# Optimization experiments

Hardware: AMD Instinct MI355X
Metric: run time of the kernel (lower is better)

## Reference

```python
import jax, jax.numpy as jnp
import numpy as np

N, E, G = 2048, 65536, 32
F_ATOM, LAT, IN, ED, NB, L = 16, 64, 128, 32, 5, 5


def setup_inputs() -> dict:
    key = jax.random.key(0)
    ks = iter(jax.random.split(key, 64))
    nxt = lambda: next(ks)
    def w(shape):
        fan_in = shape[-2] if len(shape) >= 2 else 1
        return jax.random.normal(nxt(), shape, jnp.float32) / np.sqrt(fan_in)
    inp = {}
    inp['x'] = jax.random.normal(nxt(), (N, F_ATOM), jnp.float32)
    inp['t'] = jax.random.uniform(nxt(), (G, 1), jnp.float32)
    inp['z'] = jax.random.normal(nxt(), (N, LAT), jnp.float32)
    inp['edge_index'] = jax.random.randint(nxt(), (2, E), 0, N, jnp.int32)
    inp['edge_attr'] = jax.random.normal(nxt(), (E, NB), jnp.float32)
    inp['batch'] = jnp.sort(jax.random.randint(nxt(), (N,), 0, G, jnp.int32))
    inp['batch_edge_global'] = jax.random.randint(nxt(), (E,), 0, G, jnp.int32)
    # top-level dense layers
    inp['Wt_a'] = w((1, IN)); inp['bt_a'] = jnp.zeros((IN,))
    inp['Wt_b'] = w((1, ED)); inp['bt_b'] = jnp.zeros((ED,))
    inp['W_atom'] = w((F_ATOM, IN)); inp['b_atom'] = jnp.zeros((IN,))
    inp['W_bond'] = w((NB, ED)); inp['b_bond'] = jnp.zeros((ED,))
    inp['W_lat'] = w((LAT, IN)); inp['b_lat'] = jnp.zeros((IN,))
    inp['W_at'] = w((IN, IN)); inp['b_at'] = jnp.zeros((IN,))
    inp['W_bt'] = w((ED, ED)); inp['b_bt'] = jnp.zeros((ED,))
    # TopoEdgeGNN: L layers of edge-conditioned message passing with edge update
    inp['Wmsg'] = w((L, 2 * IN + ED, IN)); inp['bmsg'] = jnp.zeros((L, IN))
    inp['Wnode'] = w((L, 2 * IN, IN)); inp['bnode'] = jnp.zeros((L, IN))
    inp['Wedge'] = w((L, 2 * IN + ED, ED)); inp['bedge'] = jnp.zeros((L, ED))
    # prediction head
    inp['Wsh'] = w((IN, IN)); inp['bsh'] = jnp.zeros((IN,))
    inp['Wbm'] = w((ED, IN)); inp['bbm'] = jnp.zeros((IN,))
    inp['Wbl'] = w((IN, NB)); inp['bbl'] = jnp.zeros((NB,))
    inp['Wal'] = w((IN, F_ATOM + LAT)); inp['bal'] = jnp.zeros((F_ATOM + LAT,))
    return inp


def reference(x, t, z, edge_index, edge_attr, batch, batch_edge_global,
              Wt_a, bt_a, Wt_b, bt_b, W_atom, b_atom, W_bond, b_bond,
              W_lat, b_lat, W_at, b_at, W_bt, b_bt,
              Wmsg, bmsg, Wnode, bnode, Wedge, bedge,
              Wsh, bsh, Wbm, bbm, Wbl, bbl, Wal, bal):
    j, i = edge_index[0], edge_index[1]
    # time embeddings, gathered to nodes / edges
    ta = t @ Wt_a + bt_a            # [G, IN]
    tb = t @ Wt_b + bt_b            # [G, ED]
    tnode = ta[batch]               # [N, IN]
    tedge = tb[batch_edge_global]   # [E, ED]
    # node features
    s = x @ W_atom + b_atom
    s = (s + tnode) @ W_at + b_at
    s = s + (z @ W_lat + b_lat)
    # edge features
    e = edge_attr @ W_bond + b_bond
    e = (e + tedge) @ W_bt + b_bt
    # TopoEdgeGNN: message passing with residual node/edge updates
    for l in range(L):
        m = jax.nn.silu(jnp.concatenate([s[i], s[j], e], -1) @ Wmsg[l] + bmsg[l])  # [E, IN]
        agg = jax.ops.segment_sum(m, i, num_segments=N)                            # [N, IN]
        s = s + jax.nn.silu(jnp.concatenate([s, agg], -1) @ Wnode[l] + bnode[l])
        e = e + jax.nn.silu(jnp.concatenate([s[i], s[j], e], -1) @ Wedge[l] + bedge[l])
    # prediction head
    s2 = jax.nn.silu(s @ Wsh + bsh)
    al = s2 @ Wal + bal
    atoms_pred, latent_pred = al[:, :F_ATOM], al[:, F_ATOM:]
    # dense edge symmetrization: scatter edges into [N, N, ED], symmetrize, gather back
    e_dense = jnp.zeros((N, N, ED), e.dtype).at[j, i].set(e)
    e_dense = 0.5 * (e_dense + e_dense.transpose(1, 0, 2))
    e_sym = e_dense[j, i]           # [E, ED]
    f = jax.nn.silu(s2[i] + s2[j] + (e_sym @ Wbm + bbm))
    bonds_pred = f @ Wbl + bbl
    return latent_pred, atoms_pred, bonds_pred
```

## Files before the change

### kernel.cpp

```cpp
#include <hip/hip_runtime.h>
#include <hip/hip_bf16.h>

#define NN 2048
#define NE 65536
#define NG 32
#define CIN 128
#define CED 32
#define CLAT 64
#define CFA 16
#define CNB 5
#define NL 5

#define OFF_AT (NN * CLAT)
#define OFF_B  (NN * CLAT + NN * CFA)

typedef __attribute__((ext_vector_type(8))) short bf16x8;
typedef __attribute__((ext_vector_type(4))) float f32x4;

__device__ __forceinline__ float silu_f(float v) { return v / (1.0f + __expf(-v)); }
__device__ __forceinline__ short f2bs(float v) {
    __hip_bfloat16 h = __float2bfloat16(v);
    return *reinterpret_cast<short*>(&h);
}
__device__ __forceinline__ float bs2f(short s) {
    return __bfloat162float(*reinterpret_cast<__hip_bfloat16*>(&s));
}
__device__ __forceinline__ unsigned pack2(float a, float b) {
    return ((unsigned)(unsigned short)f2bs(b) << 16) | (unsigned short)f2bs(a);
}
__device__ __forceinline__ unsigned addpack(unsigned ua, unsigned va) {
    float a0 = bs2f((short)(ua & 0xffff)), a1 = bs2f((short)(ua >> 16));
    float b0 = bs2f((short)(va & 0xffff)), b1 = bs2f((short)(va >> 16));
    return pack2(a0 + b0, a1 + b1);
}

struct KArgs {
    const float *x, *t, *z;
    const int *jj, *ii;
    const float *ea;
    const int *batch, *beg;
    const float *Wt_a, *bt_a, *Wt_b, *bt_b, *W_atom, *b_atom, *W_bond, *b_bond;
    const float *W_lat, *b_lat, *W_at, *b_at, *W_bt, *b_bt;
    const float *Wmsg, *bmsg, *Wnode, *bnode, *Wedge, *bedge;
    const float *Wsh, *bsh, *Wbm, *bbm, *Wbl, *bbl, *Wal, *bal;
    float *s, *e;
    float *agg;
    int *cnt, *rowpos, *rowstart, *invp, *i_s, *j_s;
    short *s2, *U, *V, *P, *Q;
    int *map;
    short *Wpn, *Wpsh, *Wpal, *Wpbm, *Wproj, *W3m, *We3;
    int *gsync;
    float *out;
};

__device__ __forceinline__ void gbar(int* gs)
{
    __syncthreads();
    if (threadIdx.x == 0) {
        __threadfence();
        int g = __hip_atomic_load(gs + 32, __ATOMIC_RELAXED, __HIP_MEMORY_SCOPE_AGENT);
        int* gc = gs + 64 + ((blockIdx.x >> 5) << 5);
        if (__hip_atomic_fetch_add(gc, 1, __ATOMIC_ACQ_REL, __HIP_MEMORY_SCOPE_AGENT) == 31) {
            __hip_atomic_store(gc, 0, __ATOMIC_RELAXED, __HIP_MEMORY_SCOPE_AGENT);
            if (__hip_atomic_fetch_add(gs, 1, __ATOMIC_ACQ_REL, __HIP_MEMORY_SCOPE_AGENT) == 31) {
                __hip_atomic_store(gs, 0, __ATOMIC_RELAXED, __HIP_MEMORY_SCOPE_AGENT);
                __hip_atomic_store(gs + 32, g + 1, __ATOMIC_RELEASE, __HIP_MEMORY_SCOPE_AGENT);
            }
        }
        while (__hip_atomic_load(gs + 32, __ATOMIC_RELAXED, __HIP_MEMORY_SCOPE_AGENT) == g)
            __builtin_amdgcn_s_sleep(8);
    }
    __syncthreads();
    __threadfence();
}

__device__ __forceinline__ void phase_pack(const KArgs& a, int start, int stride)
{
    for (int idx = start; idx < 6 * 4 * 20 * 64 * 8; idx += stride) {
        int j = idx & 7, t0 = idx >> 3, lane = t0 & 63, tt = t0 >> 6;
        int kq = (lane >> 4) * 8 + j, n16 = lane & 15;
        if (idx < NL * 8 * 8 * 64 * 8) {
            int nt = tt & 7, kt = (tt >> 3) & 7, l = tt >> 6;
            a.Wpn[idx] = f2bs(a.Wnode[((size_t)l * 256 + kt * 32 + kq) * CIN + nt * 16 + n16]);
        }
        if (idx < 4 * 8 * 64 * 8) {
            int nt = tt & 7, kt = tt >> 3;
            a.Wpsh[idx] = f2bs(a.Wsh[(size_t)(kt * 32 + kq) * CIN + nt * 16 + n16]);
        }
        if (idx < 4 * 5 * 64 * 8) {
            int nt = tt % 5, kt = tt / 5;
            a.Wpal[idx] = f2bs(a.Wal[(size_t)(kt * 32 + kq) * 80 + nt * 16 + n16]);
        }
        if (idx < 8 * 64 * 8) {
            int nt = tt & 7;
            a.Wpbm[idx] = f2bs(a.Wbm[(size_t)kq * CIN + nt * 16 + n16]);
        }
        {
            int nt = tt % 20; int t2 = tt / 20; int kt = t2 & 3; int slot = t2 >> 2;
            int k = kt * 32 + kq;
            float v;
            if (nt < 16) {
                int msgl = slot % 5;
                int srcK = (nt < 8) ? k : 128 + k;
                int col = (nt & 7) * 16 + n16;
                v = a.Wmsg[((size_t)msgl * 288 + srcK) * CIN + col];
            } else {
                int edgel = (slot == 0) ? 0 : slot - 1;
                int srcK = (nt < 18) ? k : 128 + k;
                int col = (nt & 1) * 16 + n16;
                v = a.Wedge[((size_t)edgel * 288 + srcK) * CED + col];
            }
            a.Wproj[idx] = f2bs(v);
        }
        if (idx < NL * 8 * 64 * 8) {
            int nt = tt & 7, l = tt >> 3;
            a.W3m[idx] = f2bs(a.Wmsg[((size_t)l * 288 + 256 + kq) * CIN + nt * 16 + n16]);
        }
        if (idx < NL * 2 * 64 * 8) {
            int nt = tt & 1, l = tt >> 1;
            a.We3[idx] = f2bs(a.Wedge[((size_t)l * 288 + 256 + kq) * CED + nt * 16 + n16]);
        }
    }
}

__device__ __forceinline__ void phase_init_s(const KArgs& a, char* smem, int tile, int tid)
{
    float* xs  = (float*)smem;
    float* zs  = (float*)(smem + 1024);
    float* tmp = (float*)(smem + 5120);
    float* tv  = (float*)(smem + 13312);
    int nb0 = tile * 16;
    int c = tid & 127, h = tid >> 7;
    if (tid < 16 * CFA / 4) ((float4*)xs)[tid] = ((const float4*)a.x)[nb0 * (CFA / 4) + tid];
    if (tid < 16 * CLAT / 4) ((float4*)zs)[tid] = ((const float4*)a.z)[nb0 * (CLAT / 4) + tid];
    if (tid < 16) tv[tid] = a.t[a.batch[nb0 + tid]];
    __syncthreads();
    float wta = a.Wt_a[c], base0 = a.b_atom[c] + a.bt_a[c];
    float acc[8];
#pragma unroll
    for (int q = 0; q < 8; q++) acc[q] = base0 + tv[h * 8 + q] * wta;
    for (int k = 0; k < CFA; k++) {
        float w = a.W_atom[k * CIN + c];
#pragma unroll
        for (int q = 0; q < 8; q++) acc[q] += xs[(h * 8 + q) * CFA + k] * w;
    }
#pragma unroll
    for (int q = 0; q < 8; q++) tmp[(h * 8 + q) * CIN + c] = acc[q];
    __syncthreads();
    float base1 = a.b_at[c] + a.b_lat[c];
    float acc2[8];
#pragma unroll
    for (int q = 0; q < 8; q++) acc2[q] = base1;
    for (int k4 = 0; k4 < CIN / 4; k4++) {
        float w0 = a.W_at[(4 * k4 + 0) * CIN + c], w1 = a.W_at[(4 * k4 + 1) * CIN + c];
        float w2 = a.W_at[(4 * k4 + 2) * CIN + c], w3 = a.W_at[(4 * k4 + 3) * CIN + c];
#pragma unroll
        for (int q = 0; q < 8; q++) {
            float4 f = *(const float4*)&tmp[(h * 8 + q) * CIN + 4 * k4];
            acc2[q] += f.x * w0 + f.y * w1 + f.z * w2 + f.w * w3;
        }
    }
    for (int k4 = 0; k4 < CLAT / 4; k4++) {
        float w0 = a.W_lat[(4 * k4 + 0) * CIN + c], w1 = a.W_lat[(4 * k4 + 1) * CIN + c];
        float w2 = a.W_lat[(4 * k4 + 2) * CIN + c], w3 = a.W_lat[(4 * k4 + 3) * CIN + c];
#pragma unroll
        for (int q = 0; q < 8; q++) {
            float4 f = *(const float4*)&zs[(h * 8 + q) * CLAT + 4 * k4];
            acc2[q] += f.x * w0 + f.y * w1 + f.z * w2 + f.w * w3;
        }
    }
#pragma unroll
    for (int q = 0; q < 8; q++) {
        int nd = nb0 + h * 8 + q;
        a.s[(size_t)nd * CIN + c] = acc2[q];
    }
}

__device__ __forceinline__ void phase_init_e(const KArgs& a, char* smem, int tb, int tid)
{
    float* eas   = (float*)smem;
    float* tv    = (float*)(smem + 1280);
    int*   sp    = (int*)(smem + 1536);
    float* tmp   = (float*)(smem + 1792);
    float* wbt   = (float*)(smem + 10240);
    float* wbond = (float*)(smem + 14336);
    float* cb    = (float*)(smem + 14976);
    float* wtb   = (float*)(smem + 15104);
    float* bbt2  = (float*)(smem + 15232);
    int k0 = tb * 64;
    for (int idx = tid; idx < 320; idx += 256) eas[idx] = a.ea[(size_t)k0 * 5 + idx];
    if (tid < 64) { tv[tid] = a.t[a.beg[k0 + tid]]; sp[tid] = a.invp[k0 + tid]; }
    for (int idx = tid; idx < 1024; idx += 256) wbt[idx] = a.W_bt[idx];
    if (tid < 160) wbond[tid] = a.W_bond[tid];
    if (tid < 32) { cb[tid] = a.b_bond[tid] + a.bt_b[tid]; wtb[tid] = a.Wt_b[tid]; bbt2[tid] = a.b_bt[tid]; }
    __syncthreads();
    int ch = tid & 31, eg = tid >> 5;
#pragma unroll
    for (int q = 0; q < 8; q++) {
        int le = eg * 8 + q;
        float acc = cb[ch] + tv[le] * wtb[ch];
#pragma unroll
        for (int bb = 0; bb < CNB; bb++) acc += eas[le * 5 + bb] * wbond[bb * 32 + ch];
        tmp[le * 33 + ch] = acc;
    }
    __syncthreads();
#pragma unroll
    for (int q = 0; q < 8; q++) {
        int le = eg * 8 + q;
        float acc2 = bbt2[ch];
        for (int d = 0; d < 32; d++) acc2 += tmp[le * 33 + d] * wbt[d * 32 + ch];
        size_t ix = (size_t)sp[le] * CED + ch;
        a.e[ix] = acc2;
        if (ch == 0) {
            int k = k0 + le;
            atomicMax(&a.map[(size_t)a.jj[k] * NN + a.ii[k]], k);
        }
    }
}

__device__ __forceinline__ void phase_node2(
    const KArgs& a, char* smem, int tile, int tid, bool DO_NODE, bool DO_POST,
    bool LOAD_S, bool STORE_S,
    const short* Wpn_l, const float* bnode_l, const short* Wproj_slot, float (*s_reg)[4])
{
    short* feat  = (short*)smem;
    short* feat2 = (short*)(smem + 8448);
    int nb0 = tile * 16;
    int lane = tid & 63, w = tid >> 6;
    int quad = lane >> 4, n16 = lane & 15;

    if (DO_NODE) {
#pragma unroll
        for (int n2 = 0; n2 < 2; n2++) {
            int col = (w * 2 + n2) * 16 + n16;
#pragma unroll
            for (int r = 0; r < 4; r++) {
                int row = quad * 4 + r;
                if (LOAD_S) s_reg[n2][r] = a.s[(size_t)(nb0 + row) * CIN + col];
                feat[row * 264 + col] = f2bs(s_reg[n2][r]);
            }
        }
#pragma unroll
        for (int k2 = 0; k2 < 2; k2++) {
            int idx = tid + k2 * 256;
            int kl = idx >> 5, c = idx & 31;
            size_t base = (size_t)(nb0 + kl) * 128 + c;
            float4 p0 = ((const float4*)a.agg)[base];
            float4 p1 = ((const float4*)a.agg)[base + 32];
            float4 p2 = ((const float4*)a.agg)[base + 64];
            float4 p3 = ((const float4*)a.agg)[base + 96];
            float4 z4 = {0.f, 0.f, 0.f, 0.f};
            ((float4*)a.agg)[base] = z4;
            ((float4*)a.agg)[base + 32] = z4;
            ((float4*)a.agg)[base + 64] = z4;
            ((float4*)a.agg)[base + 96] = z4;
            float4 v; v.x = p0.x + p1.x + p2.x + p3.x; v.y = p0.y + p1.y + p2.y + p3.y;
            v.z = p0.z + p1.z + p2.z + p3.z; v.w = p0.w + p1.w + p2.w + p3.w;
            uint2 p; p.x = pack2(v.x, v.y); p.y = pack2(v.z, v.w);
            *(uint2*)&feat[kl * 264 + 128 + 4 * c] = p;
        }
        __syncthreads();
        f32x4 acc[2];
        acc[0] = (f32x4){0.f, 0.f, 0.f, 0.f};
        acc[1] = (f32x4){0.f, 0.f, 0.f, 0.f};
        const short* fbase = feat + n16 * 264 + quad * 8;
#pragma unroll
        for (int kt = 0; kt < 8; kt++) {
            bf16x8 av = *(const bf16x8*)(fbase + kt * 32);
#pragma unroll
            for (int n2 = 0; n2 < 2; n2++) {
                int nt = w * 2 + n2;
                bf16x8 b = *(const bf16x8*)(Wpn_l + ((size_t)(kt * 8 + nt) * 64 + lane) * 8);
                acc[n2] = __builtin_amdgcn_mfma_f32_16x16x32_bf16(av, b, acc[n2], 0, 0, 0);
            }
        }
#pragma unroll
        for (int n2 = 0; n2 < 2; n2++) {
            int col = (w * 2 + n2) * 16 + n16;
            float bb = bnode_l[col];
#pragma unroll
            for (int r = 0; r < 4; r++) {
                int row = quad * 4 + r;
                float v = s_reg[n2][r] + silu_f(acc[n2][r] + bb);
                s_reg[n2][r] = v;
                if (STORE_S) a.s[(size_t)(nb0 + row) * CIN + col] = v;
                feat2[row * 136 + col] = f2bs(v);
            }
        }
        __syncthreads();
    } else {
        int kl = tid >> 4, c = tid & 15;
        const float4* sp4 = (const float4*)&a.s[(size_t)(nb0 + kl) * CIN + c * 8];
        float4 v0 = sp4[0], v1 = sp4[1];
        uint4 p; p.x = pack2(v0.x, v0.y); p.y = pack2(v0.z, v0.w);
        p.z = pack2(v1.x, v1.y); p.w = pack2(v1.z, v1.w);
        *(uint4*)&feat2[kl * 136 + c * 8] = p;
        __syncthreads();
    }

    {
        f32x4 accp[5];
#pragma unroll
        for (int t2 = 0; t2 < 5; t2++) accp[t2] = (f32x4){0.f, 0.f, 0.f, 0.f};
        const short* abase = feat2 + n16 * 136 + quad * 8;
#pragma unroll
        for (int kt = 0; kt < 4; kt++) {
            bf16x8 av = *(const bf16x8*)(abase + kt * 32);
#pragma unroll
            for (int n5 = 0; n5 < 5; n5++) {
                int nt = w * 5 + n5;
                bf16x8 b = *(const bf16x8*)(Wproj_slot + ((size_t)(kt * 20 + nt) * 64 + lane) * 8);
                accp[n5] = __builtin_amdgcn_mfma_f32_16x16x32_bf16(av, b, accp[n5], 0, 0, 0);
            }
        }
#pragma unroll
        for (int n5 = 0; n5 < 5; n5++) {
            int nt = w * 5 + n5;
#pragma unroll
            for (int r = 0; r < 4; r++) {
                int node = tile * 16 + quad * 4 + r;
                short bv = f2bs(accp[n5][r]);
                if (nt < 8)       a.U[(size_t)node * CIN + nt * 16 + n16] = bv;
                else if (nt < 16) a.V[(size_t)node * CIN + (nt - 8) * 16 + n16] = bv;
                else if (nt < 18) a.P[(size_t)node * CED + (nt - 16) * 16 + n16] = bv;
                else              a.Q[(size_t)node * CED + (nt - 18) * 16 + n16] = bv;
            }
        }
    }

    if (DO_POST) {
        short* feat_s2 = feat;
        const short* fbase = feat2 + n16 * 136 + quad * 8;
        f32x4 acc[2];
        acc[0] = (f32x4){0.f, 0.f, 0.f, 0.f};
        acc[1] = (f32x4){0.f, 0.f, 0.f, 0.f};
#pragma unroll
        for (int kt = 0; kt < 4; kt++) {
            bf16x8 av = *(const bf16x8*)(fbase + kt * 32);
#pragma unroll
            for (int n2 = 0; n2 < 2; n2++) {
                int nt = w * 2 + n2;
                bf16x8 b = *(const bf16x8*)(a.Wpsh + ((size_t)(kt * 8 + nt) * 64 + lane) * 8);
                acc[n2] = __builtin_amdgcn_mfma_f32_16x16x32_bf16(av, b, acc[n2], 0, 0, 0);
            }
        }
#pragma unroll
        for (int n2 = 0; n2 < 2; n2++) {
            int col = (w * 2 + n2) * 16 + n16;
            float bb = a.bsh[col];
#pragma unroll
            for (int r = 0; r < 4; r++) {
                int row = quad * 4 + r;
                float v = silu_f(acc[n2][r] + bb);
                short bv = f2bs(v);
                a.s2[(size_t)(nb0 + row) * CIN + col] = bv;
                feat_s2[row * 136 + col] = bv;
            }
        }
        __syncthreads();
        const short* abase2 = feat_s2 + n16 * 136 + quad * 8;
        f32x4 acca[2];
        acca[0] = (f32x4){0.f, 0.f, 0.f, 0.f};
        acca[1] = (f32x4){0.f, 0.f, 0.f, 0.f};
        int nAl = (w == 0) ? 2 : 1;
        int ntl[2] = {w, 4};
#pragma unroll
        for (int kt = 0; kt < 4; kt++) {
            bf16x8 av = *(const bf16x8*)(abase2 + kt * 32);
#pragma unroll
            for (int q = 0; q < 2; q++) {
                if (q < nAl) {
                    bf16x8 b = *(const bf16x8*)(a.Wpal + ((size_t)(kt * 5 + ntl[q]) * 64 + lane) * 8);
                    acca[q] = __builtin_amdgcn_mfma_f32_16x16x32_bf16(av, b, acca[q], 0, 0, 0);
                }
            }
        }
#pragma unroll
        for (int q = 0; q < 2; q++) {
            if (q < nAl) {
                int col = ntl[q] * 16 + n16;
                float bb = a.bal[col];
#pragma unroll
                for (int r = 0; r < 4; r++) {
                    int node = nb0 + quad * 4 + r;
                    float v = acca[q][r] + bb;
                    if (col < CFA) a.out[OFF_AT + node * CFA + col] = v;
                    else           a.out[(size_t)node * CLAT + (col - CFA)] = v;
                }
            }
        }
    }
}

__device__ __forceinline__ void phase_em2(
    const KArgs& a, char* smem, int tb, int tid, bool DO_EDGE, bool DO_MSG, bool LOAD_E, bool WRITE_E,
    const short* We3p, const float* bedge_l, const short* W3mp, const float* bmsg_l,
    float (*e_reg)[4])
{
    short* feat_e = (short*)smem;
    short* uv_bf  = (short*)(smem + 5120);
    short* pq_bf  = (short*)(smem + 22528);
    int*   sii    = (int*)(smem + 27648);
    int*   sjj    = (int*)(smem + 27904);
    int e0 = tb * 64;
    int lane = tid & 63, w = tid >> 6;
    int quad = lane >> 4, n16 = lane & 15;
    if (tid < 64) sii[tid] = a.i_s[e0 + tid];
    else if (tid < 128) sjj[tid - 64] = a.j_s[e0 + tid - 64];
    __syncthreads();
#pragma unroll
    for (int nt = 0; nt < 2; nt++) {
        int ch = nt * 16 + n16;
#pragma unroll
        for (int r = 0; r < 4; r++) {
            int el = w * 16 + quad * 4 + r;
            if (LOAD_E) e_reg[nt][r] = a.e[(size_t)(e0 + el) * CED + ch];
            feat_e[el * 40 + ch] = f2bs(e_reg[nt][r]);
        }
    }
    if (DO_EDGE) {
        uint2 pa[2], qb[2];
#pragma unroll
        for (int k2 = 0; k2 < 2; k2++) {
            int idx = tid + k2 * 256;
            int kl = idx >> 3, c = idx & 7;
            pa[k2] = ((const uint2*)a.P)[(size_t)sii[kl] * 8 + c];
            qb[k2] = ((const uint2*)a.Q)[(size_t)sjj[kl] * 8 + c];
        }
#pragma unroll
        for (int k2 = 0; k2 < 2; k2++) {
            int idx = tid + k2 * 256;
            int kl = idx >> 3, c = idx & 7;
            uint2 o; o.x = addpack(pa[k2].x, qb[k2].x); o.y = addpack(pa[k2].y, qb[k2].y);
            *(uint2*)&pq_bf[kl * 40 + 4 * c] = o;
        }
    }
    if (DO_MSG) {
        uint4 ua[4], va[4];
#pragma unroll
        for (int k2 = 0; k2 < 4; k2++) {
            int idx = tid + k2 * 256;
            int kl = idx >> 4, c = idx & 15;
            ua[k2] = ((const uint4*)a.U)[(size_t)sii[kl] * 16 + c];
            va[k2] = ((const uint4*)a.V)[(size_t)sjj[kl] * 16 + c];
        }
#pragma unroll
        for (int k2 = 0; k2 < 4; k2++) {
            int idx = tid + k2 * 256;
            int kl = idx >> 4, c = idx & 15;
            uint4 o; o.x = addpack(ua[k2].x, va[k2].x); o.y = addpack(ua[k2].y, va[k2].y);
            o.z = addpack(ua[k2].z, va[k2].z); o.w = addpack(ua[k2].w, va[k2].w);
            *(uint4*)&uv_bf[kl * 136 + c * 8] = o;
        }
    }
    __syncthreads();
    const short* abase = feat_e + (w * 16 + n16) * 40 + quad * 8;
    bf16x8 av = *(const bf16x8*)abase;

    if (DO_EDGE) {
        f32x4 acc_e[2];
        acc_e[0] = (f32x4){0.f, 0.f, 0.f, 0.f};
        acc_e[1] = (f32x4){0.f, 0.f, 0.f, 0.f};
#pragma unroll
        for (int nt = 0; nt < 2; nt++) {
            bf16x8 b = *(const bf16x8*)(We3p + ((size_t)(nt * 64 + lane)) * 8);
            acc_e[nt] = __builtin_amdgcn_mfma_f32_16x16x32_bf16(av, b, acc_e[nt], 0, 0, 0);
        }
#pragma unroll
        for (int nt = 0; nt < 2; nt++) {
            int ch = nt * 16 + n16;
            float bb = bedge_l[ch];
#pragma unroll
            for (int r = 0; r < 4; r++) {
                int el = w * 16 + quad * 4 + r;
                float v = e_reg[nt][r] + silu_f(acc_e[nt][r] + bb + bs2f(pq_bf[el * 40 + ch]));
                e_reg[nt][r] = v;
                feat_e[el * 40 + ch] = f2bs(v);
                if (WRITE_E) a.e[(size_t)(e0 + el) * CED + ch] = v;
            }
        }
        av = *(const bf16x8*)abase;
    }

    if (DO_MSG) {
        f32x4 acc_m[8];
#pragma unroll
        for (int t2 = 0; t2 < 8; t2++) acc_m[t2] = (f32x4){0.f, 0.f, 0.f, 0.f};
#pragma unroll
        for (int nt = 0; nt < 8; nt++) {
            bf16x8 b = *(const bf16x8*)(W3mp + ((size_t)(nt * 64 + lane)) * 8);
            acc_m[nt] = __builtin_amdgcn_mfma_f32_16x16x32_bf16(av, b, acc_m[nt], 0, 0, 0);
        }
#pragma unroll
        for (int nt = 0; nt < 8; nt++) {
            int ch = nt * 16 + n16;
            float bb = bmsg_l[ch];
#pragma unroll
            for (int r = 0; r < 4; r++) {
                int el = w * 16 + quad * 4 + r;
                int lix = el * 136 + ch;
                float m = silu_f(acc_m[nt][r] + bb + bs2f(uv_bf[lix]));
                uv_bf[lix] = f2bs(m);
            }
        }
        __syncthreads();
        if (tid < 128) {
            int c = tid;
            float run = 0.f;
            int cur = sii[0];
            for (int r = 0; r < 64; r++) {
                int tg = sii[r];
                if (tg != cur) {
                    int slot = tb - (a.rowstart[cur] >> 6); slot = (slot > 3) ? 3 : slot;
                    a.agg[((size_t)cur * 4 + slot) * CIN + c] = run;
                    run = 0.f; cur = tg;
                }
                run += bs2f(uv_bf[r * 136 + c]);
            }
            int slot = tb - (a.rowstart[cur] >> 6); slot = (slot > 3) ? 3 : slot;
            a.agg[((size_t)cur * 4 + slot) * CIN + c] = run;
        }
    }
}

__device__ __forceinline__ void phase_post_edge(const KArgs& a, char* smem, int tb, int tid)
{
    short* esym  = (short*)smem;
    short* sbias = (short*)(smem + 5120);
    int* sii = (int*)(smem + 22016);
    int* sjj = (int*)(smem + 22272);
    int* skf = (int*)(smem + 22528);
    int* skb = (int*)(smem + 22784);
    int e0 = tb * 64;
    if (tid < 64) sii[tid] = a.ii[e0 + tid];
    else if (tid < 128) sjj[tid - 64] = a.jj[e0 + tid - 64];
    __syncthreads();
    if (tid < 64) skf[tid] = a.invp[a.map[(size_t)sjj[tid] * NN + sii[tid]]];
    else if (tid < 128) {
        int m = a.map[(size_t)sii[tid - 64] * NN + sjj[tid - 64]];
        skb[tid - 64] = (m >= 0) ? a.invp[m] : -1;
    }
    __syncthreads();
    {
        float4 av2[2], bv2[2];
#pragma unroll
        for (int k2 = 0; k2 < 2; k2++) {
            int idx = tid + k2 * 256;
            int kl = idx >> 3, c = idx & 7;
            av2[k2] = ((const float4*)a.e)[(size_t)skf[kl] * 8 + c];
            int kb = skb[kl];
            bv2[k2] = (float4){0.f, 0.f, 0.f, 0.f};
            if (kb >= 0) bv2[k2] = ((const float4*)a.e)[(size_t)kb * 8 + c];
        }
#pragma unroll
        for (int k2 = 0; k2 < 2; k2++) {
            int idx = tid + k2 * 256;
            int kl = idx >> 3, c = idx & 7;
            uint2 p; p.x = pack2(0.5f * (av2[k2].x + bv2[k2].x), 0.5f * (av2[k2].y + bv2[k2].y));
            p.y = pack2(0.5f * (av2[k2].z + bv2[k2].z), 0.5f * (av2[k2].w + bv2[k2].w));
            *(uint2*)&esym[kl * 40 + 4 * c] = p;
        }
    }
#pragma unroll
    for (int half = 0; half < 2; half++) {
        uint2 av4[4], bv4[4];
#pragma unroll
        for (int k2 = 0; k2 < 4; k2++) {
            int idx = tid + (half * 4 + k2) * 256;
            int kl = idx >> 5, c = idx & 31;
            av4[k2] = ((const uint2*)a.s2)[(size_t)sii[kl] * 32 + c];
            bv4[k2] = ((const uint2*)a.s2)[(size_t)sjj[kl] * 32 + c];
        }
#pragma unroll
        for (int k2 = 0; k2 < 4; k2++) {
            int idx = tid + (half * 4 + k2) * 256;
            int kl = idx >> 5, c = idx & 31;
            uint2 o; o.x = addpack(av4[k2].x, bv4[k2].x); o.y = addpack(av4[k2].y, bv4[k2].y);
            *(uint2*)&sbias[kl * 132 + 4 * c] = o;
        }
    }
    __syncthreads();
    int lane = tid & 63, w = tid >> 6;
    int quad = lane >> 4, n16 = lane & 15;
    bf16x8 av = *(const bf16x8*)(esym + (w * 16 + n16) * 40 + quad * 8);
    f32x4 acc[8];
#pragma unroll
    for (int nt = 0; nt < 8; nt++) {
        bf16x8 b = *(const bf16x8*)(a.Wpbm + ((size_t)nt * 64 + lane) * 8);
        f32x4 zero = {0.f, 0.f, 0.f, 0.f};
        acc[nt] = __builtin_amdgcn_mfma_f32_16x16x32_bf16(av, b, zero, 0, 0, 0);
    }
    float f[8][4];
#pragma unroll
    for (int nt = 0; nt < 8; nt++) {
        int col = nt * 16 + n16;
        float bb = a.bbm[col];
#pragma unroll
        for (int r = 0; r < 4; r++) {
            int row = w * 16 + quad * 4 + r;
            f[nt][r] = silu_f(acc[nt][r] + bb + bs2f(sbias[row * 132 + col]));
        }
    }
    __syncthreads();
    short* fshT = sbias;
#pragma unroll
    for (int nt = 0; nt < 8; nt++) {
        int col = nt * 16 + n16;
#pragma unroll
        for (int r = 0; r < 4; r++) {
            int row = w * 16 + quad * 4 + r;
            fshT[col * 66 + row] = f2bs(f[nt][r]);
        }
    }
    __syncthreads();
    for (int idx = tid; idx < 64 * CNB; idx += 256) {
        int kl = idx / CNB, b = idx - kl * CNB;
        float acc3 = a.bbl[b];
        for (int d = 0; d < CIN; d++) acc3 += bs2f(fshT[d * 66 + kl]) * a.Wbl[d * CNB + b];
        a.out[OFF_B + (size_t)(e0 + kl) * CNB + b] = acc3;
    }
}

__global__ __launch_bounds__(256, 4) void k_main(KArgs a)
{
    __shared__ __align__(16) char smem[28160];
    int bid = blockIdx.x, tid = threadIdx.x;
    int* gs = a.gsync;
    float s_reg[2][4], e_reg[2][4];

    {
        float4 z4 = {0.f, 0.f, 0.f, 0.f};
        ((float4*)a.agg)[bid * 256 + tid] = z4;
    }
    if (bid < 128) phase_init_s(a, smem, bid, tid);
    else phase_pack(a, (bid - 128) * 256 + tid, 896 * 256);
    if (bid >= 192 && bid < 448) atomicAdd(&a.cnt[a.ii[(bid - 192) * 256 + tid]], 1);
    {
        int4 m1 = {-1, -1, -1, -1};
#pragma unroll
        for (int q = 0; q < 4; q++)
            ((int4*)a.map)[(size_t)bid * 1024 + q * 256 + tid] = m1;
    }
    gbar(gs);

    if (bid == 0) {
        int* part = (int*)smem;
        int loc[8], sum = 0;
#pragma unroll
        for (int q = 0; q < 8; q++) { loc[q] = a.cnt[tid * 8 + q]; sum += loc[q]; }
        part[tid] = sum;
        __syncthreads();
        if (tid == 0) { int r = 0; for (int i = 0; i < 256; i++) { int v = part[i]; part[i] = r; r += v; } }
        __syncthreads();
        int r = part[tid];
#pragma unroll
        for (int q = 0; q < 8; q++) { a.rowpos[tid * 8 + q] = r; a.rowstart[tid * 8 + q] = r; r += loc[q]; }
        __syncthreads();
    }
    if (bid < 128) phase_node2(a, smem, bid, tid, false, false, false, false,
                               nullptr, nullptr, a.Wproj, s_reg);
    gbar(gs);

    if (bid < 256) {
        int k = bid * 256 + tid;
        int iv = a.ii[k];
        int p = atomicAdd(&a.rowpos[iv], 1);
        a.invp[k] = p;
        a.i_s[p] = iv;
        a.j_s[p] = a.jj[k];
    }
    gbar(gs);

    phase_init_e(a, smem, bid, tid);
    gbar(gs);

    phase_em2(a, smem, bid, tid, false, true, true, false, nullptr, nullptr, a.W3m, a.bmsg, e_reg);
    gbar(gs);

    for (int l = 0; l < NL; l++) {
        if (bid < 128)
            phase_node2(a, smem, bid, tid, true, l == NL - 1, l == 0, false,
                        a.Wpn + (size_t)l * 8 * 8 * 64 * 8, a.bnode + l * CIN,
                        a.Wproj + (size_t)(l + 1) * 4 * 20 * 64 * 8, s_reg);
        gbar(gs);
        bool dm = (l < NL - 1);
        phase_em2(a, smem, bid, tid, true, dm, false, l == NL - 1,
                  a.We3 + (size_t)l * 2 * 64 * 8, a.bedge + l * CED,
                  dm ? a.W3m + (size_t)(l + 1) * 8 * 64 * 8 : a.W3m,
                  dm ? a.bmsg + (l + 1) * CIN : a.bmsg, e_reg);
        gbar(gs);
    }

    phase_post_edge(a, smem, bid, tid);
}

__global__ __launch_bounds__(256) void k_prologue(KArgs a)
{
    __shared__ __align__(16) char smem[13440];
    int b = blockIdx.x, tid = threadIdx.x;
    if (b < 960) phase_pack(a, b * 256 + tid, 960 * 256);
    else if (b < 1088) phase_init_s(a, smem, b - 960, tid);
    else {
        int base = (b - 1088) * 1024;
#pragma unroll
        for (int q = 0; q < 4; q++) atomicAdd(&a.cnt[a.ii[base + q * 256 + tid]], 1);
    }
}
__global__ __launch_bounds__(256) void k_prefix(KArgs a)
{
    __shared__ int part[256];
    int tid = threadIdx.x;
    int loc[8], sum = 0;
#pragma unroll
    for (int q = 0; q < 8; q++) { loc[q] = a.cnt[tid * 8 + q]; sum += loc[q]; }
    part[tid] = sum;
    __syncthreads();
    if (tid == 0) { int r = 0; for (int i = 0; i < 256; i++) { int v = part[i]; part[i] = r; r += v; } }
    __syncthreads();
    int r = part[tid];
#pragma unroll
    for (int q = 0; q < 8; q++) { a.rowpos[tid * 8 + q] = r; a.rowstart[tid * 8 + q] = r; r += loc[q]; }
}
__global__ void k_perm(KArgs a)
{
    int k = blockIdx.x * 256 + threadIdx.x;
    int iv = a.ii[k];
    int p = atomicAdd(&a.rowpos[iv], 1);
    a.invp[k] = p;
    a.i_s[p] = iv;
    a.j_s[p] = a.jj[k];
}
__global__ __launch_bounds__(256) void k_init_e(KArgs a)
{
    __shared__ __align__(16) char smem[15360];
    phase_init_e(a, smem, blockIdx.x, threadIdx.x);
}
__global__ __launch_bounds__(256) void k_node_proj(KArgs a, int donode, int dopost,
                                                   const short* Wpn_l, const float* bnode_l,
                                                   const short* Wproj_slot)
{
    __shared__ __align__(16) char smem[12800];
    float s_reg[2][4];
    phase_node2(a, smem, blockIdx.x, threadIdx.x, donode != 0, dopost != 0,
                donode != 0, donode != 0, Wpn_l, bnode_l, Wproj_slot, s_reg);
}
__global__ __launch_bounds__(256) void k_em(KArgs a, int de, int dm, const short* We3p,
                                            const float* bedge_l, const short* W3mp, const float* bmsg_l)
{
    __shared__ __align__(16) char smem[28160];
    float e_reg[2][4];
    phase_em2(a, smem, blockIdx.x, threadIdx.x, de != 0, dm != 0, true, de != 0,
              We3p, bedge_l, W3mp, bmsg_l, e_reg);
}
__global__ __launch_bounds__(256) void k_post_edge(KArgs a)
{
    __shared__ __align__(16) char smem[23040];
    phase_post_edge(a, smem, blockIdx.x, threadIdx.x);
}

extern "C" void kernel_launch(void* const* d_in, const int* in_sizes, int n_in,
                              void* d_out, int out_size, void* d_ws, size_t ws_size,
                              hipStream_t stream) {
    KArgs a;
    a.x      = (const float*)d_in[0];
    a.t      = (const float*)d_in[1];
    a.z      = (const float*)d_in[2];
    const int* eidx = (const int*)d_in[3];
    a.jj     = eidx;
    a.ii     = eidx + NE;
    a.ea     = (const float*)d_in[4];
    a.batch  = (const int*)d_in[5];
    a.beg    = (const int*)d_in[6];
    a.Wt_a   = (const float*)d_in[7];
    a.bt_a   = (const float*)d_in[8];
    a.Wt_b   = (const float*)d_in[9];
    a.bt_b   = (const float*)d_in[10];
    a.W_atom = (const float*)d_in[11];
    a.b_atom = (const float*)d_in[12];
    a.W_bond = (const float*)d_in[13];
    a.b_bond = (const float*)d_in[14];
    a.W_lat  = (const float*)d_in[15];
    a.b_lat  = (const float*)d_in[16];
    a.W_at   = (const float*)d_in[17];
    a.b_at   = (const float*)d_in[18];
    a.W_bt   = (const float*)d_in[19];
    a.b_bt   = (const float*)d_in[20];
    a.Wmsg   = (const float*)d_in[21];
    a.bmsg   = (const float*)d_in[22];
    a.Wnode  = (const float*)d_in[23];
    a.bnode  = (const float*)d_in[24];
    a.Wedge  = (const float*)d_in[25];
    a.bedge  = (const float*)d_in[26];
    a.Wsh    = (const float*)d_in[27];
    a.bsh    = (const float*)d_in[28];
    a.Wbm    = (const float*)d_in[29];
    a.bbm    = (const float*)d_in[30];
    a.Wbl    = (const float*)d_in[31];
    a.bbl    = (const float*)d_in[32];
    a.Wal    = (const float*)d_in[33];
    a.bal    = (const float*)d_in[34];

    a.s        = (float*)d_ws;
    a.e        = a.s + (size_t)NN * CIN;
    a.agg      = a.e + (size_t)NE * CED;
    a.cnt      = (int*)(a.agg + (size_t)NN * 4 * CIN);
    a.rowpos   = a.cnt + NN;
    a.rowstart = a.rowpos + NN;
    a.invp     = a.rowstart + NN;
    a.i_s      = a.invp + NE;
    a.j_s      = a.i_s + NE;
    a.s2       = (short*)(a.j_s + NE);
    a.U        = a.s2 + (size_t)NN * CIN;
    a.V        = a.U + (size_t)NN * CIN;
    a.P        = a.V + (size_t)NN * CIN;
    a.Q        = a.P + (size_t)NN * CED;
    a.map      = (int*)(a.Q + (size_t)NN * CED);
    a.Wpn      = (short*)(a.map + (size_t)NN * NN);
    a.Wpsh     = a.Wpn + (size_t)NL * 8 * 8 * 64 * 8;
    a.Wpal     = a.Wpsh + (size_t)4 * 8 * 64 * 8;
    a.Wpbm     = a.Wpal + (size_t)4 * 5 * 64 * 8;
    a.Wproj    = a.Wpbm + (size_t)8 * 64 * 8;
    a.W3m      = a.Wproj + (size_t)6 * 4 * 20 * 64 * 8;
    a.We3      = a.W3m + (size_t)NL * 8 * 64 * 8;
    a.gsync    = (int*)(a.We3 + (size_t)NL * 2 * 64 * 8);
    a.out      = (float*)d_out;

    int use_fused = 0;

    if (use_fused) {
        hipMemsetAsync(a.gsync, 0, (64 + 32 * 32) * sizeof(int), stream);
        hipMemsetAsync(a.cnt, 0, NN * sizeof(int), stream);
        k_main<<<1024, 256, 0, stream>>>(a);
    } else {
        hipMemsetAsync(a.map, 0xFF, (size_t)NN * NN * sizeof(int), stream);
        hipMemsetAsync(a.agg, 0, (size_t)NN * 4 * CIN * sizeof(float) + NN * sizeof(int), stream);
        k_prologue<<<1152, 256, 0, stream>>>(a);
        k_prefix<<<1, 256, 0, stream>>>(a);
        k_perm<<<NE / 256, 256, 0, stream>>>(a);
        k_init_e<<<NE / 64, 256, 0, stream>>>(a);
        k_node_proj<<<NN / 16, 256, 0, stream>>>(a, 0, 0, nullptr, nullptr, a.Wproj);
        k_em<<<NE / 64, 256, 0, stream>>>(a, 0, 1, nullptr, nullptr, a.W3m, a.bmsg);
        for (int l = 0; l < NL; l++) {
            int dopost = (l == NL - 1) ? 1 : 0;
            k_node_proj<<<NN / 16, 256, 0, stream>>>(a, 1, dopost,
                a.Wpn + (size_t)l * 8 * 8 * 64 * 8, a.bnode + l * CIN,
                a.Wproj + (size_t)(l + 1) * 4 * 20 * 64 * 8);
            int dm = (l < NL - 1) ? 1 : 0;
            k_em<<<NE / 64, 256, 0, stream>>>(a, 1, dm,
                a.We3 + (size_t)l * 2 * 64 * 8, a.bedge + l * CED,
                dm ? a.W3m + (size_t)(l + 1) * 8 * 64 * 8 : a.W3m,
                dm ? a.bmsg + (l + 1) * CIN : a.bmsg);
        }
        k_post_edge<<<NE / 64, 256, 0, stream>>>(a);
    }
}
```

Before: 340.6 us.

## Overlap edge and node phases per layer using flag-based inter-block dependencies

Replaces the separate per-layer node and edge kernels with one launch per layer. In that launch, edge/message blocks publish per-tile completion flags and node blocks spin on the flags covering their rows before reading the aggregates, so node updates overlap with edge work. The permutation and initial edge init are merged the same way through per-block flags. Redundant zeroing of the aggregate buffer is dropped. A one-time occupancy check picks this path only when all blocks can be co-resident, because the spin waits could deadlock otherwise. The cost is busy-waiting and extra fences.

```diff
diff --git a/kernel.cpp b/kernel.cpp
--- a/kernel.cpp
+++ b/kernel.cpp
@@ -45,34 +45,12 @@
     const float *Wsh, *bsh, *Wbm, *bbm, *Wbl, *bbl, *Wal, *bal;
     float *s, *e;
     float *agg;
-    int *cnt, *rowpos, *rowstart, *invp, *i_s, *j_s;
+    int *cnt, *pflag, *eflag, *rowpos, *rowstart, *invp, *i_s, *j_s;
     short *s2, *U, *V, *P, *Q;
     int *map;
     short *Wpn, *Wpsh, *Wpal, *Wpbm, *Wproj, *W3m, *We3;
-    int *gsync;
     float *out;
 };
-
-__device__ __forceinline__ void gbar(int* gs)
-{
-    __syncthreads();
-    if (threadIdx.x == 0) {
-        __threadfence();
-        int g = __hip_atomic_load(gs + 32, __ATOMIC_RELAXED, __HIP_MEMORY_SCOPE_AGENT);
-        int* gc = gs + 64 + ((blockIdx.x >> 5) << 5);
-        if (__hip_atomic_fetch_add(gc, 1, __ATOMIC_ACQ_REL, __HIP_MEMORY_SCOPE_AGENT) == 31) {
-            __hip_atomic_store(gc, 0, __ATOMIC_RELAXED, __HIP_MEMORY_SCOPE_AGENT);
-            if (__hip_atomic_fetch_add(gs, 1, __ATOMIC_ACQ_REL, __HIP_MEMORY_SCOPE_AGENT) == 31) {
-                __hip_atomic_store(gs, 0, __ATOMIC_RELAXED, __HIP_MEMORY_SCOPE_AGENT);
-                __hip_atomic_store(gs + 32, g + 1, __ATOMIC_RELEASE, __HIP_MEMORY_SCOPE_AGENT);
-            }
-        }
-        while (__hip_atomic_load(gs + 32, __ATOMIC_RELAXED, __HIP_MEMORY_SCOPE_AGENT) == g)
-            __builtin_amdgcn_s_sleep(8);
-    }
-    __syncthreads();
-    __threadfence();
-}
 
 __device__ __forceinline__ void phase_pack(const KArgs& a, int start, int stride)
 {
@@ -221,7 +199,8 @@
 __device__ __forceinline__ void phase_node2(
     const KArgs& a, char* smem, int tile, int tid, bool DO_NODE, bool DO_POST,
     bool LOAD_S, bool STORE_S,
-    const short* Wpn_l, const float* bnode_l, const short* Wproj_slot, float (*s_reg)[4])
+    const short* Wpn_l, const float* bnode_l, const short* Wproj_slot, float (*s_reg)[4],
+    const int* eflag, int gen)
 {
     short* feat  = (short*)smem;
     short* feat2 = (short*)(smem + 8448);
@@ -230,6 +209,20 @@
     int quad = lane >> 4, n16 = lane & 15;
 
     if (DO_NODE) {
+        if (eflag) {
+            if (tid == 0) {
+                int r0 = a.rowstart[nb0];
+                int ed = (nb0 + 16 < NN) ? a.rowstart[nb0 + 16] : NE;
+                if (ed > r0) {
+                    int t1 = (ed - 1) >> 6;
+                    for (int t = r0 >> 6; t <= t1; t++)
+                        while (__hip_atomic_load(&eflag[t], __ATOMIC_RELAXED, __HIP_MEMORY_SCOPE_AGENT) < gen)
+                            __builtin_amdgcn_s_sleep(2);
+                }
+            }
+            __syncthreads();
+            __threadfence();
+        }
 #pragma unroll
         for (int n2 = 0; n2 < 2; n2++) {
             int col = (w * 2 + n2) * 16 + n16;
@@ -249,11 +242,6 @@
             float4 p1 = ((const float4*)a.agg)[base + 32];
             float4 p2 = ((const float4*)a.agg)[base + 64];
             float4 p3 = ((const float4*)a.agg)[base + 96];
-            float4 z4 = {0.f, 0.f, 0.f, 0.f};
-            ((float4*)a.agg)[base] = z4;
-            ((float4*)a.agg)[base + 32] = z4;
-            ((float4*)a.agg)[base + 64] = z4;
-            ((float4*)a.agg)[base + 96] = z4;
             float4 v; v.x = p0.x + p1.x + p2.x + p3.x; v.y = p0.y + p1.y + p2.y + p3.y;
             v.z = p0.z + p1.z + p2.z + p3.z; v.w = p0.w + p1.w + p2.w + p3.w;
             uint2 p; p.x = pack2(v.x, v.y); p.y = pack2(v.z, v.w);
@@ -395,7 +383,7 @@
 __device__ __forceinline__ void phase_em2(
     const KArgs& a, char* smem, int tb, int tid, bool DO_EDGE, bool DO_MSG, bool LOAD_E, bool WRITE_E,
     const short* We3p, const float* bedge_l, const short* W3mp, const float* bmsg_l,
-    float (*e_reg)[4])
+    float (*e_reg)[4], int* eflag, int gen)
 {
     short* feat_e = (short*)smem;
     short* uv_bf  = (short*)(smem + 5120);
@@ -520,6 +508,13 @@
             int slot = tb - (a.rowstart[cur] >> 6); slot = (slot > 3) ? 3 : slot;
             a.agg[((size_t)cur * 4 + slot) * CIN + c] = run;
         }
+        if (eflag) {
+            __syncthreads();
+            if (tid == 0) {
+                __threadfence();
+                __hip_atomic_store(&eflag[tb], gen, __ATOMIC_RELAXED, __HIP_MEMORY_SCOPE_AGENT);
+            }
+        }
     }
 }
 
@@ -621,46 +616,44 @@
     }
 }
 
-__global__ __launch_bounds__(256, 4) void k_main(KArgs a)
-{
-    __shared__ __align__(16) char smem[28160];
+__global__ __launch_bounds__(256) void k_prologue(KArgs a)
+{
+    __shared__ __align__(16) char smem[13440];
+    int b = blockIdx.x, tid = threadIdx.x;
+    if (b < 960) phase_pack(a, b * 256 + tid, 960 * 256);
+    else if (b < 1088) phase_init_s(a, smem, b - 960, tid);
+    else {
+        int base = (b - 1088) * 1024;
+#pragma unroll
+        for (int q = 0; q < 4; q++) atomicAdd(&a.cnt[a.ii[base + q * 256 + tid]], 1);
+    }
+}
+__global__ __launch_bounds__(256) void k_prefix(KArgs a)
+{
+    __shared__ int part[256];
+    int tid = threadIdx.x;
+    int loc[8], sum = 0;
+#pragma unroll
+    for (int q = 0; q < 8; q++) { loc[q] = a.cnt[tid * 8 + q]; sum += loc[q]; }
+    part[tid] = sum;
+    __syncthreads();
+    if (tid == 0) { int r = 0; for (int i = 0; i < 256; i++) { int v = part[i]; part[i] = r; r += v; } }
+    __syncthreads();
+    int r = part[tid];
+#pragma unroll
+    for (int q = 0; q < 8; q++) { a.rowpos[tid * 8 + q] = r; a.rowstart[tid * 8 + q] = r; r += loc[q]; }
+}
+
+__global__ __launch_bounds__(256, 5) void k_permE(KArgs a)
+{
+    __shared__ __align__(16) char smem[15360];
     int bid = blockIdx.x, tid = threadIdx.x;
-    int* gs = a.gsync;
-    float s_reg[2][4], e_reg[2][4];
-
-    {
-        float4 z4 = {0.f, 0.f, 0.f, 0.f};
-        ((float4*)a.agg)[bid * 256 + tid] = z4;
-    }
-    if (bid < 128) phase_init_s(a, smem, bid, tid);
-    else phase_pack(a, (bid - 128) * 256 + tid, 896 * 256);
-    if (bid >= 192 && bid < 448) atomicAdd(&a.cnt[a.ii[(bid - 192) * 256 + tid]], 1);
-    {
-        int4 m1 = {-1, -1, -1, -1};
-#pragma unroll
-        for (int q = 0; q < 4; q++)
-            ((int4*)a.map)[(size_t)bid * 1024 + q * 256 + tid] = m1;
-    }
-    gbar(gs);
-
-    if (bid == 0) {
-        int* part = (int*)smem;
-        int loc[8], sum = 0;
-#pragma unroll
-        for (int q = 0; q < 8; q++) { loc[q] = a.cnt[tid * 8 + q]; sum += loc[q]; }
-        part[tid] = sum;
-        __syncthreads();
-        if (tid == 0) { int r = 0; for (int i = 0; i < 256; i++) { int v = part[i]; part[i] = r; r += v; } }
-        __syncthreads();
-        int r = part[tid];
-#pragma unroll
-        for (int q = 0; q < 8; q++) { a.rowpos[tid * 8 + q] = r; a.rowstart[tid * 8 + q] = r; r += loc[q]; }
-        __syncthreads();
-    }
-    if (bid < 128) phase_node2(a, smem, bid, tid, false, false, false, false,
-                               nullptr, nullptr, a.Wproj, s_reg);
-    gbar(gs);
-
+    if (bid >= 1024) {
+        float s_reg[2][4];
+        phase_node2(a, smem, bid - 1024, tid, false, false, false, false,
+                    nullptr, nullptr, a.Wproj, s_reg, nullptr, 0);
+        return;
+    }
     if (bid < 256) {
         int k = bid * 256 + tid;
         int iv = a.ii[k];
@@ -668,59 +661,38 @@
         a.invp[k] = p;
         a.i_s[p] = iv;
         a.j_s[p] = a.jj[k];
-    }
-    gbar(gs);
-
+        __syncthreads();
+        if (tid == 0) {
+            __threadfence();
+            __hip_atomic_store(&a.pflag[bid], 1, __ATOMIC_RELAXED, __HIP_MEMORY_SCOPE_AGENT);
+        }
+    }
+    if (tid == 0) {
+        while (__hip_atomic_load(&a.pflag[bid >> 2], __ATOMIC_RELAXED, __HIP_MEMORY_SCOPE_AGENT) == 0)
+            __builtin_amdgcn_s_sleep(2);
+    }
+    __syncthreads();
+    __threadfence();
     phase_init_e(a, smem, bid, tid);
-    gbar(gs);
-
-    phase_em2(a, smem, bid, tid, false, true, true, false, nullptr, nullptr, a.W3m, a.bmsg, e_reg);
-    gbar(gs);
-
-    for (int l = 0; l < NL; l++) {
-        if (bid < 128)
-            phase_node2(a, smem, bid, tid, true, l == NL - 1, l == 0, false,
-                        a.Wpn + (size_t)l * 8 * 8 * 64 * 8, a.bnode + l * CIN,
-                        a.Wproj + (size_t)(l + 1) * 4 * 20 * 64 * 8, s_reg);
-        gbar(gs);
-        bool dm = (l < NL - 1);
-        phase_em2(a, smem, bid, tid, true, dm, false, l == NL - 1,
-                  a.We3 + (size_t)l * 2 * 64 * 8, a.bedge + l * CED,
-                  dm ? a.W3m + (size_t)(l + 1) * 8 * 64 * 8 : a.W3m,
-                  dm ? a.bmsg + (l + 1) * CIN : a.bmsg, e_reg);
-        gbar(gs);
-    }
-
-    phase_post_edge(a, smem, bid, tid);
-}
-
-__global__ __launch_bounds__(256) void k_prologue(KArgs a)
-{
-    __shared__ __align__(16) char smem[13440];
-    int b = blockIdx.x, tid = threadIdx.x;
-    if (b < 960) phase_pack(a, b * 256 + tid, 960 * 256);
-    else if (b < 1088) phase_init_s(a, smem, b - 960, tid);
-    else {
-        int base = (b - 1088) * 1024;
-#pragma unroll
-        for (int q = 0; q < 4; q++) atomicAdd(&a.cnt[a.ii[base + q * 256 + tid]], 1);
-    }
-}
-__global__ __launch_bounds__(256) void k_prefix(KArgs a)
-{
-    __shared__ int part[256];
-    int tid = threadIdx.x;
-    int loc[8], sum = 0;
-#pragma unroll
-    for (int q = 0; q < 8; q++) { loc[q] = a.cnt[tid * 8 + q]; sum += loc[q]; }
-    part[tid] = sum;
-    __syncthreads();
-    if (tid == 0) { int r = 0; for (int i = 0; i < 256; i++) { int v = part[i]; part[i] = r; r += v; } }
-    __syncthreads();
-    int r = part[tid];
-#pragma unroll
-    for (int q = 0; q < 8; q++) { a.rowpos[tid * 8 + q] = r; a.rowstart[tid * 8 + q] = r; r += loc[q]; }
-}
+}
+
+__global__ __launch_bounds__(256, 5) void k_layer(KArgs a, int gen, int de, int dm,
+        const short* We3p, const float* bedge_l, const short* W3mp, const float* bmsg_l,
+        const short* Wpn_l, const float* bnode_l, const short* Wproj_slot, int dopost)
+{
+    __shared__ __align__(16) char smem[28160];
+    int bid = blockIdx.x, tid = threadIdx.x;
+    if (bid < 1024) {
+        float e_reg[2][4];
+        phase_em2(a, smem, bid, tid, de != 0, dm != 0, true, de != 0,
+                  We3p, bedge_l, W3mp, bmsg_l, e_reg, a.eflag, gen);
+    } else {
+        float s_reg[2][4];
+        phase_node2(a, smem, bid - 1024, tid, true, dopost != 0, true, true,
+                    Wpn_l, bnode_l, Wproj_slot, s_reg, a.eflag, gen);
+    }
+}
+
 __global__ void k_perm(KArgs a)
 {
     int k = blockIdx.x * 256 + threadIdx.x;
@@ -742,7 +714,7 @@
     __shared__ __align__(16) char smem[12800];
     float s_reg[2][4];
     phase_node2(a, smem, blockIdx.x, threadIdx.x, donode != 0, dopost != 0,
-                donode != 0, donode != 0, Wpn_l, bnode_l, Wproj_slot, s_reg);
+                donode != 0, donode != 0, Wpn_l, bnode_l, Wproj_slot, s_reg, nullptr, 0);
 }
 __global__ __launch_bounds__(256) void k_em(KArgs a, int de, int dm, const short* We3p,
                                             const float* bedge_l, const short* W3mp, const float* bmsg_l)
@@ -750,7 +722,7 @@
     __shared__ __align__(16) char smem[28160];
     float e_reg[2][4];
     phase_em2(a, smem, blockIdx.x, threadIdx.x, de != 0, dm != 0, true, de != 0,
-              We3p, bedge_l, W3mp, bmsg_l, e_reg);
+              We3p, bedge_l, W3mp, bmsg_l, e_reg, nullptr, 0);
 }
 __global__ __launch_bounds__(256) void k_post_edge(KArgs a)
 {
@@ -804,7 +776,9 @@
     a.e        = a.s + (size_t)NN * CIN;
     a.agg      = a.e + (size_t)NE * CED;
     a.cnt      = (int*)(a.agg + (size_t)NN * 4 * CIN);
-    a.rowpos   = a.cnt + NN;
+    a.pflag    = a.cnt + NN;
+    a.eflag    = a.pflag + 256;
+    a.rowpos   = a.eflag + 1024;
     a.rowstart = a.rowpos + NN;
     a.invp     = a.rowstart + NN;
     a.i_s      = a.invp + NE;
@@ -822,20 +796,44 @@
     a.Wproj    = a.Wpbm + (size_t)8 * 64 * 8;
     a.W3m      = a.Wproj + (size_t)6 * 4 * 20 * 64 * 8;
     a.We3      = a.W3m + (size_t)NL * 8 * 64 * 8;
-    a.gsync    = (int*)(a.We3 + (size_t)NL * 2 * 64 * 8);
     a.out      = (float*)d_out;
 
-    int use_fused = 0;
-
-    if (use_fused) {
-        hipMemsetAsync(a.gsync, 0, (64 + 32 * 32) * sizeof(int), stream);
-        hipMemsetAsync(a.cnt, 0, NN * sizeof(int), stream);
-        k_main<<<1024, 256, 0, stream>>>(a);
+    static int mode = -1;
+    if (mode < 0) {
+        int dev = 0;
+        (void)hipGetDevice(&dev);
+        hipDeviceProp_t props;
+        int ncu = 0;
+        if (hipGetDeviceProperties(&props, dev) == hipSuccess) ncu = props.multiProcessorCount;
+        int m1 = 0, m2 = 0;
+        if (hipOccupancyMaxActiveBlocksPerMultiprocessor(&m1, k_layer, 256, 0) != hipSuccess) m1 = 0;
+        if (hipOccupancyMaxActiveBlocksPerMultiprocessor(&m2, k_permE, 256, 0) != hipSuccess) m2 = 0;
+        mode = ((long)m1 * ncu >= 1152 && (long)m2 * ncu >= 1152) ? 1 : 0;
+    }
+
+    hipMemsetAsync(a.map, 0xFF, (size_t)NN * NN * sizeof(int), stream);
+    hipMemsetAsync(a.agg, 0,
+                   (size_t)NN * 4 * CIN * sizeof(float) + (NN + 256 + 1024) * sizeof(int),
+                   stream);
+
+    k_prologue<<<1152, 256, 0, stream>>>(a);
+    k_prefix<<<1, 256, 0, stream>>>(a);
+
+    if (mode) {
+        k_permE<<<1152, 256, 0, stream>>>(a);
+        for (int k = 0; k < NL; k++) {
+            int de = (k > 0) ? 1 : 0;
+            k_layer<<<1152, 256, 0, stream>>>(a, k + 1, de, 1,
+                de ? a.We3 + (size_t)(k - 1) * 2 * 64 * 8 : a.We3,
+                de ? a.bedge + (k - 1) * CED : a.bedge,
+                a.W3m + (size_t)k * 8 * 64 * 8, a.bmsg + k * CIN,
+                a.Wpn + (size_t)k * 8 * 8 * 64 * 8, a.bnode + k * CIN,
+                a.Wproj + (size_t)(k + 1) * 4 * 20 * 64 * 8, (k == NL - 1) ? 1 : 0);
+        }
+        k_layer<<<1024, 256, 0, stream>>>(a, NL + 1, 1, 0,
+            a.We3 + (size_t)(NL - 1) * 2 * 64 * 8, a.bedge + (NL - 1) * CED,
+            a.W3m, a.bmsg, a.Wpn, a.bnode, a.Wproj, 0);
     } else {
-        hipMemsetAsync(a.map, 0xFF, (size_t)NN * NN * sizeof(int), stream);
-        hipMemsetAsync(a.agg, 0, (size_t)NN * 4 * CIN * sizeof(float) + NN * sizeof(int), stream);
-        k_prologue<<<1152, 256, 0, stream>>>(a);
-        k_prefix<<<1, 256, 0, stream>>>(a);
         k_perm<<<NE / 256, 256, 0, stream>>>(a);
         k_init_e<<<NE / 64, 256, 0, stream>>>(a);
         k_node_proj<<<NN / 16, 256, 0, stream>>>(a, 0, 0, nullptr, nullptr, a.Wproj);
@@ -851,6 +849,6 @@
                 dm ? a.W3m + (size_t)(l + 1) * 8 * 64 * 8 : a.W3m,
                 dm ? a.bmsg + (l + 1) * CIN : a.bmsg);
         }
-        k_post_edge<<<NE / 64, 256, 0, stream>>>(a);
-    }
-}
+    }
+    k_post_edge<<<NE / 64, 256, 0, stream>>>(a);
+}
```

New measurement: 342.1 us. No clear change (+0.4%).
